# Kernel tuning notes

Hardware: AMD Instinct MI355X
Metric: run time of the kernel (lower is better)

## Reference

```python
import jax, jax.numpy as jnp
import numpy as np

EMBED_DIM = 1024
NUM_HEADS = 16
HEAD_DIM = EMBED_DIM // NUM_HEADS
B, SQ, SKV = 2, 2048, 2048


def setup_inputs() -> dict:
    key = jax.random.key(0)
    ks = jax.random.split(key, 12)
    s = 1.0 / np.sqrt(EMBED_DIM)
    inp = {
        "query": jax.random.normal(ks[0], (B, SQ, EMBED_DIM), jnp.float32),
        "key": jax.random.normal(ks[1], (B, SKV, EMBED_DIM), jnp.float32),
        "value": jax.random.normal(ks[2], (B, SKV, EMBED_DIM), jnp.float32),
        "Wq": jax.random.normal(ks[3], (EMBED_DIM, EMBED_DIM), jnp.float32) * s,
        "bq": jnp.zeros((EMBED_DIM,), jnp.float32),
        "Wk": jax.random.normal(ks[4], (EMBED_DIM, EMBED_DIM), jnp.float32) * s,
        "bk": jnp.zeros((EMBED_DIM,), jnp.float32),
        "Wv": jax.random.normal(ks[5], (EMBED_DIM, EMBED_DIM), jnp.float32) * s,
        "bv": jnp.zeros((EMBED_DIM,), jnp.float32),
        "Wo": jax.random.normal(ks[6], (EMBED_DIM, EMBED_DIM), jnp.float32) * s,
        "bo": jnp.zeros((EMBED_DIM,), jnp.float32),
        "ln_gamma": jnp.ones((EMBED_DIM,), jnp.float32),
        "ln_beta": jnp.zeros((EMBED_DIM,), jnp.float32),
    }
    return inp


def reference(query, key, value, Wq, bq, Wk, bk, Wv, bv, Wo, bo, ln_gamma, ln_beta):
    b, sq, d = query.shape
    skv = key.shape[1]
    residual = query
    # projections -> [b, h, s, hd]
    Q = (query @ Wq + bq).reshape(b, sq, NUM_HEADS, HEAD_DIM).transpose(0, 2, 1, 3)
    K = (key @ Wk + bk).reshape(b, skv, NUM_HEADS, HEAD_DIM).transpose(0, 2, 1, 3)
    V = (value @ Wv + bv).reshape(b, skv, NUM_HEADS, HEAD_DIM).transpose(0, 2, 1, 3)
    scores = jnp.einsum("bhqd,bhkd->bhqk", Q, K) / jnp.sqrt(jnp.float32(HEAD_DIM)).astype(Q.dtype)
    attn = jax.nn.softmax(scores, axis=-1)  # dropout identity in eval
    attended = jnp.einsum("bhqk,bhkd->bhqd", attn, V)
    attended = attended.transpose(0, 2, 1, 3).reshape(b, sq, d)
    out = attended @ Wo + bo
    x = out + residual
    mu = jnp.mean(x, axis=-1, keepdims=True)
    var = jnp.var(x, axis=-1, keepdims=True)
    return (x - mu) / jnp.sqrt(var + 1e-5) * ln_gamma + ln_beta
```

## Files before the change

kernel.cpp:

```cpp
#include <hip/hip_runtime.h>

#define EMBED 1024
#define NHEAD 16
#define HDIM  64
#define BATCH 2
#define SEQ   2048
#define ROWS  (BATCH*SEQ)

typedef __bf16 bf16x8 __attribute__((ext_vector_type(8)));
typedef float  f32x4  __attribute__((ext_vector_type(4)));
typedef float  f32x16 __attribute__((ext_vector_type(16)));
typedef unsigned short u16x8 __attribute__((ext_vector_type(8)));
typedef unsigned short u16x4 __attribute__((ext_vector_type(4)));

__device__ __forceinline__ unsigned short f2bf(float f) {
    unsigned int u = __float_as_uint(f);
    u += 0x7FFFu + ((u >> 16) & 1u);
    return (unsigned short)(u >> 16);
}
__device__ __forceinline__ f32x4 zero4() { f32x4 z = {0.f, 0.f, 0.f, 0.f}; return z; }

__device__ __forceinline__ unsigned int cvtpk_bf16(float lo, float hi) {
    unsigned int r;
    asm("v_cvt_pk_bf16_f32 %0, %1, %2" : "=v"(r) : "v"(lo), "v"(hi));
    return r;
}
__device__ __forceinline__ void pl32swap(unsigned int &a, unsigned int &b) {
    asm("v_permlane32_swap_b32 %0, %1" : "+v"(a), "+v"(b));
}
__device__ __forceinline__ float exp2_hw(float x) {
    float r;
    asm("v_exp_f32 %0, %1" : "=v"(r) : "v"(x));
    return r;
}

__device__ __forceinline__ void gl_lds16(const unsigned short* g, unsigned short* l) {
    __builtin_amdgcn_global_load_lds(
        (const __attribute__((address_space(1))) void*)g,
        (__attribute__((address_space(3))) void*)l, 16, 0, 0);
}

__global__ __launch_bounds__(256) void cvt3_kernel(const float* __restrict__ q,
                                                   const float* __restrict__ k,
                                                   const float* __restrict__ v,
                                                   unsigned short* __restrict__ qo,
                                                   unsigned short* __restrict__ ko,
                                                   unsigned short* __restrict__ vo) {
    const float* in; unsigned short* out;
    if (blockIdx.y == 0)      { in = q; out = qo; }
    else if (blockIdx.y == 1) { in = k; out = ko; }
    else                      { in = v; out = vo; }
    int i = (blockIdx.x * 256 + threadIdx.x) * 4;
    float4 vv = *(const float4*)(in + i);
    u16x4 o = {f2bf(vv.x), f2bf(vv.y), f2bf(vv.z), f2bf(vv.w)};
    *(u16x4*)(out + i) = o;
}

__global__ __launch_bounds__(256) void transpose4_kernel(const float* __restrict__ w0,
                                                         const float* __restrict__ w1,
                                                         const float* __restrict__ w2,
                                                         const float* __restrict__ w3,
                                                         unsigned short* __restrict__ o0,
                                                         unsigned short* __restrict__ o1,
                                                         unsigned short* __restrict__ o2,
                                                         unsigned short* __restrict__ o3) {
    const float* in; unsigned short* out;
    if (blockIdx.z == 0)      { in = w0; out = o0; }
    else if (blockIdx.z == 1) { in = w1; out = o1; }
    else if (blockIdx.z == 2) { in = w2; out = o2; }
    else                      { in = w3; out = o3; }
    __shared__ float tile[32][33];
    int tx = threadIdx.x, ty = threadIdx.y;
    int x = blockIdx.x * 32 + tx;
    int y0 = blockIdx.y * 32 + ty;
#pragma unroll
    for (int r = 0; r < 4; ++r)
        tile[ty + 8 * r][tx] = in[(size_t)(y0 + 8 * r) * EMBED + x];
    __syncthreads();
    int ox = blockIdx.y * 32 + tx;
    int oy = blockIdx.x * 32 + ty;
#pragma unroll
    for (int r = 0; r < 4; ++r)
        out[(size_t)(oy + 8 * r) * EMBED + ox] = f2bf(tile[tx][ty + 8 * r]);
}

__global__ __launch_bounds__(256, 2) void gemm_qkv_kernel(
    const unsigned short* __restrict__ qb, const unsigned short* __restrict__ kb,
    const unsigned short* __restrict__ vb,
    const unsigned short* __restrict__ Wqt, const unsigned short* __restrict__ Wkt,
    const unsigned short* __restrict__ Wvt,
    const float* __restrict__ bq, const float* __restrict__ bk, const float* __restrict__ bv,
    unsigned short* __restrict__ Qp, unsigned short* __restrict__ Kp,
    unsigned short* __restrict__ Vtb) {
    __shared__ unsigned short smem[24576];
    const unsigned short *A, *Bt; const float* bias; unsigned short* outp; int mode; float osc;
    if (blockIdx.z == 0)      { A = qb; Bt = Wqt; bias = bq; outp = Qp;  mode = 0; osc = 0.18033688f; }
    else if (blockIdx.z == 1) { A = kb; Bt = Wkt; bias = bk; outp = Kp;  mode = 0; osc = 1.0f; }
    else                      { A = vb; Bt = Wvt; bias = bv; outp = Vtb; mode = 1; osc = 1.0f; }

    const int t = threadIdx.x;
    const int m0 = blockIdx.x * 128, n0 = blockIdx.y * 128;
    const int wave = t >> 6, lane = t & 63;
    const int wr = wave >> 1, wc = wave & 1;
    const int lm = lane & 15, lq = lane >> 4;
    const int sr = t >> 2;
    const int csrc = (t & 3) ^ ((sr >> 1) & 3);
    const int pa = lq ^ ((lm >> 1) & 3);

    const unsigned short* gA = A + (size_t)(m0 + sr) * EMBED + csrc * 8;
    const unsigned short* gB = Bt + (size_t)(n0 + sr) * EMBED + csrc * 8;

    f32x4 acc[4][4];
#pragma unroll
    for (int i = 0; i < 4; ++i)
#pragma unroll
        for (int j = 0; j < 4; ++j) acc[i][j] = zero4();

#define QKV_STAGE(SOFF)                                                      \
    gl_lds16(gA,              smem + (SOFF) + wave * 512);                   \
    gl_lds16(gA + 64 * EMBED, smem + (SOFF) + 2048 + wave * 512);            \
    gl_lds16(gB,              smem + 12288 + (SOFF) + wave * 512);           \
    gl_lds16(gB + 64 * EMBED, smem + 12288 + (SOFF) + 2048 + wave * 512);    \
    gA += 32; gB += 32;

#define QKV_COMP(COFF)                                                                 \
    {                                                                                  \
        bf16x8 af[4], bfr[4];                                                          \
        _Pragma("unroll")                                                              \
        for (int i = 0; i < 4; ++i)                                                    \
            af[i] = *(const bf16x8*)&smem[(COFF) + (wr * 64 + i * 16 + lm) * 32 + pa * 8]; \
        _Pragma("unroll")                                                              \
        for (int j = 0; j < 4; ++j)                                                    \
            bfr[j] = *(const bf16x8*)&smem[12288 + (COFF) + (wc * 64 + j * 16 + lm) * 32 + pa * 8]; \
        _Pragma("unroll")                                                              \
        for (int i = 0; i < 4; ++i)                                                    \
            _Pragma("unroll")                                                          \
            for (int j = 0; j < 4; ++j)                                                \
                acc[i][j] = __builtin_amdgcn_mfma_f32_16x16x32_bf16(af[i], bfr[j], acc[i][j], 0, 0, 0); \
    }

    QKV_STAGE(0)
    QKV_STAGE(4096)

    for (int g = 0; g < 10; ++g) {
        asm volatile("s_waitcnt vmcnt(4)" ::: "memory");
        __builtin_amdgcn_s_barrier();
        QKV_STAGE(8192)
        QKV_COMP(0)
        asm volatile("s_waitcnt vmcnt(4)" ::: "memory");
        __builtin_amdgcn_s_barrier();
        QKV_STAGE(0)
        QKV_COMP(4096)
        asm volatile("s_waitcnt vmcnt(4)" ::: "memory");
        __builtin_amdgcn_s_barrier();
        QKV_STAGE(4096)
        QKV_COMP(8192)
    }
    asm volatile("s_waitcnt vmcnt(4)" ::: "memory");
    __builtin_amdgcn_s_barrier();
    QKV_COMP(0)
    asm volatile("s_waitcnt vmcnt(0)" ::: "memory");
    __builtin_amdgcn_s_barrier();
    QKV_COMP(4096)

    const int row = t >> 2, seg = t & 3;
    if (mode == 0) {
#pragma unroll
        for (int p = 0; p < 2; ++p) {
            __syncthreads();
            if (wr == p) {
#pragma unroll
                for (int i = 0; i < 4; ++i)
#pragma unroll
                    for (int j = 0; j < 4; ++j) {
                        float bn = bias[n0 + wc * 64 + j * 16 + lm];
                        int nl = wc * 64 + j * 16 + lm;
#pragma unroll
                        for (int r = 0; r < 4; ++r)
                            smem[(i * 16 + lq * 4 + r) * 136 + nl] =
                                f2bf((acc[i][j][r] + bn) * osc);
                    }
            }
            __syncthreads();
            int m = m0 + p * 64 + row;
            int b = m >> 11, sI = m & 2047;
            int ncol = n0 + seg * 32;
            int h = ncol >> 6, hd0 = ncol & 63;
            unsigned short* dst = outp + (((size_t)((b * NHEAD + h) * SEQ + sI)) << 6) + hd0;
            const unsigned short* src = smem + row * 136 + seg * 32;
            *(u16x8*)(dst)      = *(const u16x8*)(src);
            *(u16x8*)(dst + 8)  = *(const u16x8*)(src + 8);
            *(u16x8*)(dst + 16) = *(const u16x8*)(src + 16);
            *(u16x8*)(dst + 24) = *(const u16x8*)(src + 24);
        }
    } else {
#pragma unroll
        for (int p = 0; p < 2; ++p) {
            __syncthreads();
            if (wc == p) {
#pragma unroll
                for (int i = 0; i < 4; ++i)
#pragma unroll
                    for (int j = 0; j < 4; ++j) {
                        float bn = bias[n0 + p * 64 + j * 16 + lm];
                        u16x4 pw = {f2bf(acc[i][j][0] + bn), f2bf(acc[i][j][1] + bn),
                                    f2bf(acc[i][j][2] + bn), f2bf(acc[i][j][3] + bn)};
                        *(u16x4*)&smem[(j * 16 + lm) * 136 + wr * 64 + i * 16 + lq * 4] = pw;
                    }
            }
            __syncthreads();
            int n = n0 + p * 64 + row;
            int h = n >> 6, hd = n & 63;
            int b = m0 >> 11;
            int s0 = (m0 & 2047) + seg * 32;
            unsigned short* dst = outp + ((size_t)((b * NHEAD + h) * HDIM + hd)) * SEQ + s0;
            const unsigned short* src = smem + row * 136 + seg * 32;
            *(u16x8*)(dst)      = *(const u16x8*)(src);
            *(u16x8*)(dst + 8)  = *(const u16x8*)(src + 8);
            *(u16x8*)(dst + 16) = *(const u16x8*)(src + 16);
            *(u16x8*)(dst + 24) = *(const u16x8*)(src + 24);
        }
    }
#undef QKV_STAGE
#undef QKV_COMP
}

__global__ __launch_bounds__(256, 2) void gemm_o_kernel(
    const unsigned short* __restrict__ att, const unsigned short* __restrict__ Wot,
    const float* __restrict__ bo, float* __restrict__ xbuf,
    const float* __restrict__ residual) {
    __shared__ unsigned short smem[18432];
    const int t = threadIdx.x;
    const int m0 = blockIdx.x * 64, n0 = blockIdx.y * 128;
    const int wave = t >> 6, lane = t & 63;
    const int lm = lane & 15, lq = lane >> 4;
    const int sr = t >> 2;
    const int csrc = (t & 3) ^ ((sr >> 1) & 3);
    const int pa = lq ^ ((lm >> 1) & 3);

    const unsigned short* gA = att + (size_t)(m0 + sr) * EMBED + csrc * 8;
    const unsigned short* gB = Wot + (size_t)(n0 + sr) * EMBED + csrc * 8;

    f32x4 acc[4][2];
#pragma unroll
    for (int i = 0; i < 4; ++i)
#pragma unroll
        for (int j = 0; j < 2; ++j) acc[i][j] = zero4();

#define O_STAGE(SA, SB)                                                  \
    gl_lds16(gA,              smem + (SA) + wave * 512);                 \
    gl_lds16(gB,              smem + 6144 + (SB) + wave * 512);          \
    gl_lds16(gB + 64 * EMBED, smem + 6144 + (SB) + 2048 + wave * 512);   \
    gA += 32; gB += 32;

#define O_COMP(SA, SB)                                                                \
    {                                                                                 \
        bf16x8 af[4], bfr[2];                                                         \
        _Pragma("unroll")                                                             \
        for (int i = 0; i < 4; ++i)                                                   \
            af[i] = *(const bf16x8*)&smem[(SA) + (i * 16 + lm) * 32 + pa * 8];        \
        _Pragma("unroll")                                                             \
        for (int j = 0; j < 2; ++j)                                                   \
            bfr[j] = *(const bf16x8*)&smem[6144 + (SB) + (wave * 32 + j * 16 + lm) * 32 + pa * 8]; \
        _Pragma("unroll")                                                             \
        for (int i = 0; i < 4; ++i)                                                   \
            _Pragma("unroll")                                                         \
            for (int j = 0; j < 2; ++j)                                               \
                acc[i][j] = __builtin_amdgcn_mfma_f32_16x16x32_bf16(af[i], bfr[j], acc[i][j], 0, 0, 0); \
    }

    O_STAGE(0, 0)
    O_STAGE(2048, 4096)

    for (int g = 0; g < 10; ++g) {
        asm volatile("s_waitcnt vmcnt(3)" ::: "memory");
        __builtin_amdgcn_s_barrier();
        O_STAGE(4096, 8192)
        O_COMP(0, 0)
        asm volatile("s_waitcnt vmcnt(3)" ::: "memory");
        __builtin_amdgcn_s_barrier();
        O_STAGE(0, 0)
        O_COMP(2048, 4096)
        asm volatile("s_waitcnt vmcnt(3)" ::: "memory");
        __builtin_amdgcn_s_barrier();
        O_STAGE(2048, 4096)
        O_COMP(4096, 8192)
    }
    asm volatile("s_waitcnt vmcnt(3)" ::: "memory");
    __builtin_amdgcn_s_barrier();
    O_COMP(0, 0)
    asm volatile("s_waitcnt vmcnt(0)" ::: "memory");
    __builtin_amdgcn_s_barrier();
    O_COMP(2048, 4096)

#pragma unroll
    for (int i = 0; i < 4; ++i)
#pragma unroll
        for (int j = 0; j < 2; ++j) {
            int n = n0 + wave * 32 + j * 16 + lm;
            float bn = bo[n];
#pragma unroll
            for (int r = 0; r < 4; ++r) {
                int m = m0 + i * 16 + lq * 4 + r;
                size_t idx = (size_t)m * EMBED + n;
                xbuf[idx] = acc[i][j][r] + bn + residual[idx];
            }
        }
#undef O_STAGE
#undef O_COMP
}

__global__ __launch_bounds__(512, 4) void attn_kernel(const unsigned short* __restrict__ Qp,
                                                      const unsigned short* __restrict__ Kp,
                                                      const unsigned short* __restrict__ Vt,
                                                      unsigned short* __restrict__ att) {
    __shared__ unsigned short KV[32768];
    unsigned short* Ks = KV;
    unsigned short* Vs = KV + 16384;
    const int t = threadIdx.x;
    const int bx = blockIdx.x;
    const int bh = bx & 31;
    const int b = bh >> 4, h = bh & 15;
    const int q0 = (bx >> 5) * 128;
    const unsigned short* Qh = Qp + (size_t)bh * SEQ * HDIM;
    const unsigned short* Kh = Kp + (size_t)bh * SEQ * HDIM;
    const unsigned short* Vh = Vt + (size_t)bh * HDIM * SEQ;
    const int wave = t >> 6, lane = t & 63;
    const int g = wave >> 2, ws = wave & 3;
    const int ln31 = lane & 31, halfl = lane >> 5;

    bf16x8 qf[4];
    {
        const unsigned short* qptr = Qh + (size_t)(q0 + ws * 32 + ln31) * HDIM + halfl * 8;
#pragma unroll
        for (int s = 0; s < 4; ++s) qf[s] = *(const bf16x8*)(qptr + s * 16);
    }

    const int f0 = t >> 6, m0_ = t & 31, hh0 = (t >> 5) & 1;
    const unsigned short* gK0 = Kh + (size_t)((f0 >> 2) * 32 + m0_) * HDIM + (f0 & 3) * 16 + hh0 * 8;
    const unsigned short* gV0 = Vh + (size_t)((f0 >> 2) * 32 + m0_) * SEQ + (f0 & 3) * 16 + hh0 * 8;

#define ATTN_STAGE(NBO)                                                   \
    gl_lds16(gK0,             Ks + (NBO) + wave * 512);                   \
    gl_lds16(gK0 + 64 * HDIM, Ks + (NBO) + 4096 + wave * 512);            \
    gl_lds16(gV0,             Vs + (NBO) + wave * 512);                   \
    gl_lds16(gV0 + 64,        Vs + (NBO) + 4096 + wave * 512);            \
    gK0 += 128 * HDIM; gV0 += 128;

    ATTN_STAGE(0)
    ATTN_STAGE(8192)

    f32x16 OFFS;
#pragma unroll
    for (int r = 0; r < 16; ++r) OFFS[r] = -17.312340f;

    f32x16 Oa[2];
#pragma unroll
    for (int mo = 0; mo < 2; ++mo)
#pragma unroll
        for (int r = 0; r < 16; ++r) Oa[mo][r] = 0.f;
    float rpA = 0.f, rpB = 0.f, rpC = 0.f, rpD = 0.f;

    for (int kt = 0; kt < 16; ++kt) {
        if (kt < 15) { asm volatile("s_waitcnt vmcnt(4)" ::: "memory"); }
        else         { asm volatile("s_waitcnt vmcnt(0)" ::: "memory"); }
        __builtin_amdgcn_s_barrier();
        const int cbo = (kt & 1) * 8192 + g * 4096;

#pragma unroll
        for (int mt = 0; mt < 2; ++mt) {
            f32x16 S;
            __builtin_amdgcn_s_setprio(1);
            {
                bf16x8 af = *(const bf16x8*)&Ks[cbo + (mt * 4 + 0) * 512 + halfl * 256 + ln31 * 8];
                S = __builtin_amdgcn_mfma_f32_32x32x16_bf16(af, qf[0], OFFS, 0, 0, 0);
            }
#pragma unroll
            for (int s = 1; s < 4; ++s) {
                bf16x8 af = *(const bf16x8*)&Ks[cbo + (mt * 4 + s) * 512 + halfl * 256 + ln31 * 8];
                S = __builtin_amdgcn_mfma_f32_32x32x16_bf16(af, qf[s], S, 0, 0, 0);
            }
            __builtin_amdgcn_s_setprio(0);

#pragma unroll
            for (int rg = 0; rg < 4; ++rg) {
                float p0 = exp2_hw(S[rg * 4 + 0]);
                float p1 = exp2_hw(S[rg * 4 + 1]);
                float p2 = exp2_hw(S[rg * 4 + 2]);
                float p3 = exp2_hw(S[rg * 4 + 3]);
                S[rg * 4 + 0] = p0; rpA += p0;
                S[rg * 4 + 1] = p1; rpB += p1;
                S[rg * 4 + 2] = p2; rpC += p2;
                S[rg * 4 + 3] = p3; rpD += p3;
            }

            __builtin_amdgcn_s_setprio(1);
#pragma unroll
            for (int p = 0; p < 2; ++p) {
                unsigned int a0 = cvtpk_bf16(S[8 * p + 0], S[8 * p + 1]);
                unsigned int a1 = cvtpk_bf16(S[8 * p + 2], S[8 * p + 3]);
                unsigned int b0 = cvtpk_bf16(S[8 * p + 4], S[8 * p + 5]);
                unsigned int b1 = cvtpk_bf16(S[8 * p + 6], S[8 * p + 7]);
                pl32swap(a0, b0);
                pl32swap(a1, b1);
                union { unsigned int u[4]; bf16x8 v; } bp;
                bp.u[0] = a0; bp.u[1] = a1; bp.u[2] = b0; bp.u[3] = b1;
                const int sp = mt * 2 + p;
#pragma unroll
                for (int mo = 0; mo < 2; ++mo) {
                    bf16x8 av = *(const bf16x8*)&Vs[cbo + (mo * 4 + sp) * 512 + halfl * 256 + ln31 * 8];
                    Oa[mo] = __builtin_amdgcn_mfma_f32_32x32x16_bf16(av, bp.v, Oa[mo], 0, 0, 0);
                }
            }
            __builtin_amdgcn_s_setprio(0);
        }

        if (kt < 14) {
            __builtin_amdgcn_s_barrier();
            const int nbo = (kt & 1) * 8192;
            ATTN_STAGE(nbo)
        }
    }
#undef ATTN_STAGE

    float lsum = (rpA + rpB) + (rpC + rpD);
    unsigned int la = __float_as_uint(lsum), lb = __float_as_uint(lsum);
    pl32swap(la, lb);
    float ltot = __uint_as_float(la) + __uint_as_float(lb);

    __syncthreads();
    float* shO = (float*)KV;
    float* shL = (float*)KV + 128 * 68;
    const int qr = ws * 32 + ln31;
    if (g == 1) {
#pragma unroll
        for (int mo = 0; mo < 2; ++mo)
#pragma unroll
            for (int rg = 0; rg < 4; ++rg) {
                float4 v;
                v.x = Oa[mo][rg * 4 + 0]; v.y = Oa[mo][rg * 4 + 1];
                v.z = Oa[mo][rg * 4 + 2]; v.w = Oa[mo][rg * 4 + 3];
                *(float4*)&shO[qr * 68 + mo * 32 + rg * 8 + halfl * 4] = v;
            }
        shL[qr] = ltot;
    }
    __syncthreads();
    if (g == 0) {
        float inv = 1.f / (ltot + shL[qr]);
        unsigned short* orow = att + (size_t)(b * SEQ + q0 + qr) * EMBED + h * HDIM;
#pragma unroll
        for (int mo = 0; mo < 2; ++mo)
#pragma unroll
            for (int rg = 0; rg < 4; ++rg) {
                float4 v = *(const float4*)&shO[qr * 68 + mo * 32 + rg * 8 + halfl * 4];
                u16x4 ow = {f2bf((Oa[mo][rg * 4 + 0] + v.x) * inv),
                            f2bf((Oa[mo][rg * 4 + 1] + v.y) * inv),
                            f2bf((Oa[mo][rg * 4 + 2] + v.z) * inv),
                            f2bf((Oa[mo][rg * 4 + 3] + v.w) * inv)};
                *(u16x4*)&orow[mo * 32 + rg * 8 + halfl * 4] = ow;
            }
    }
}

__global__ __launch_bounds__(256) void ln_kernel(const float* __restrict__ x,
                                                 const float* __restrict__ gamma,
                                                 const float* __restrict__ beta,
                                                 float* __restrict__ out) {
    __shared__ float red[8];
    const int row = blockIdx.x, t = threadIdx.x;
    float4 v = *(const float4*)(x + (size_t)row * EMBED + t * 4);
    float s = v.x + v.y + v.z + v.w;
    float ss = v.x * v.x + v.y * v.y + v.z * v.z + v.w * v.w;
#pragma unroll
    for (int o = 1; o < 64; o <<= 1) {
        s += __shfl_xor(s, o);
        ss += __shfl_xor(ss, o);
    }
    int wave = t >> 6, lane = t & 63;
    if (lane == 0) { red[wave] = s; red[4 + wave] = ss; }
    __syncthreads();
    s = red[0] + red[1] + red[2] + red[3];
    ss = red[4] + red[5] + red[6] + red[7];
    float mu = s * (1.f / EMBED);
    float var = ss * (1.f / EMBED) - mu * mu;
    float rstd = rsqrtf(var + 1e-5f);
    float4 g = *(const float4*)(gamma + t * 4);
    float4 bb = *(const float4*)(beta + t * 4);
    float4 o;
    o.x = (v.x - mu) * rstd * g.x + bb.x;
    o.y = (v.y - mu) * rstd * g.y + bb.y;
    o.z = (v.z - mu) * rstd * g.z + bb.z;
    o.w = (v.w - mu) * rstd * g.w + bb.w;
    *(float4*)(out + (size_t)row * EMBED + t * 4) = o;
}

extern "C" void kernel_launch(void* const* d_in, const int* in_sizes, int n_in,
                              void* d_out, int out_size, void* d_ws, size_t ws_size,
                              hipStream_t stream) {
    const float* query = (const float*)d_in[0];
    const float* key_  = (const float*)d_in[1];
    const float* value = (const float*)d_in[2];
    const float* Wq = (const float*)d_in[3];
    const float* bq = (const float*)d_in[4];
    const float* Wk = (const float*)d_in[5];
    const float* bk = (const float*)d_in[6];
    const float* Wv = (const float*)d_in[7];
    const float* bv = (const float*)d_in[8];
    const float* Wo = (const float*)d_in[9];
    const float* bo = (const float*)d_in[10];
    const float* gamma = (const float*)d_in[11];
    const float* beta  = (const float*)d_in[12];

    char* ws = (char*)d_ws;
    const size_t MB = 1024 * 1024;
    unsigned short* qb  = (unsigned short*)(ws + 0);
    unsigned short* kb  = (unsigned short*)(ws + 8 * MB);
    unsigned short* vb  = (unsigned short*)(ws + 16 * MB);
    unsigned short* Wqt = (unsigned short*)(ws + 24 * MB);
    unsigned short* Wkt = (unsigned short*)(ws + 26 * MB);
    unsigned short* Wvt = (unsigned short*)(ws + 28 * MB);
    unsigned short* Wot = (unsigned short*)(ws + 30 * MB);
    unsigned short* Qp  = (unsigned short*)(ws + 32 * MB);
    unsigned short* Kp  = (unsigned short*)(ws + 40 * MB);
    unsigned short* Vtb = (unsigned short*)(ws + 48 * MB);
    unsigned short* att = (unsigned short*)(ws + 0);
    float*          xbuf = (float*)(ws + 8 * MB);

    cvt3_kernel<<<dim3(4096, 3), 256, 0, stream>>>(query, key_, value, qb, kb, vb);
    transpose4_kernel<<<dim3(32, 32, 4), dim3(32, 8), 0, stream>>>(Wq, Wk, Wv, Wo, Wqt, Wkt, Wvt, Wot);

    gemm_qkv_kernel<<<dim3(32, 8, 3), 256, 0, stream>>>(qb, kb, vb, Wqt, Wkt, Wvt,
                                                        bq, bk, bv, Qp, Kp, Vtb);

    attn_kernel<<<dim3(512), 512, 0, stream>>>(Qp, Kp, Vtb, att);

    gemm_o_kernel<<<dim3(64, 8), 256, 0, stream>>>(att, Wot, bo, xbuf, query);
    ln_kernel<<<ROWS, 256, 0, stream>>>(xbuf, gamma, beta, (float*)d_out);
}
```

Baseline: 224.9 us.

## Split-K the output projection GEMM and fold bias/residual into LayerNorm

The output projection GEMM is split into two K halves via a z grid dimension, doubling the block count from 512 to 1024 so the GPU's compute units have more blocks to run. Each half writes raw partial sums to a separate fp32 buffer, and the LayerNorm kernel now adds both partials, the bias and the residual. This adds an extra 16 MB fp32 write plus read of partials. Separately, the input conversion kernel handles 8 elements per thread with wider stores.

```diff
diff --git a/kernel.cpp b/kernel.cpp
--- a/kernel.cpp
+++ b/kernel.cpp
@@ -50,10 +50,12 @@
     if (blockIdx.y == 0)      { in = q; out = qo; }
     else if (blockIdx.y == 1) { in = k; out = ko; }
     else                      { in = v; out = vo; }
-    int i = (blockIdx.x * 256 + threadIdx.x) * 4;
-    float4 vv = *(const float4*)(in + i);
-    u16x4 o = {f2bf(vv.x), f2bf(vv.y), f2bf(vv.z), f2bf(vv.w)};
-    *(u16x4*)(out + i) = o;
+    int i = (blockIdx.x * 256 + threadIdx.x) * 8;
+    float4 a = *(const float4*)(in + i);
+    float4 b = *(const float4*)(in + i + 4);
+    u16x8 o = {f2bf(a.x), f2bf(a.y), f2bf(a.z), f2bf(a.w),
+               f2bf(b.x), f2bf(b.y), f2bf(b.z), f2bf(b.w)};
+    *(u16x8*)(out + i) = o;
 }
 
 __global__ __launch_bounds__(256) void transpose4_kernel(const float* __restrict__ w0,
@@ -227,19 +229,20 @@
 
 __global__ __launch_bounds__(256, 2) void gemm_o_kernel(
     const unsigned short* __restrict__ att, const unsigned short* __restrict__ Wot,
-    const float* __restrict__ bo, float* __restrict__ xbuf,
-    const float* __restrict__ residual) {
+    float* __restrict__ xbuf0, float* __restrict__ xbuf1) {
     __shared__ unsigned short smem[18432];
     const int t = threadIdx.x;
     const int m0 = blockIdx.x * 64, n0 = blockIdx.y * 128;
+    const int kz = blockIdx.z;
+    float* outp = kz ? xbuf1 : xbuf0;
     const int wave = t >> 6, lane = t & 63;
     const int lm = lane & 15, lq = lane >> 4;
     const int sr = t >> 2;
     const int csrc = (t & 3) ^ ((sr >> 1) & 3);
     const int pa = lq ^ ((lm >> 1) & 3);
 
-    const unsigned short* gA = att + (size_t)(m0 + sr) * EMBED + csrc * 8;
-    const unsigned short* gB = Wot + (size_t)(n0 + sr) * EMBED + csrc * 8;
+    const unsigned short* gA = att + (size_t)(m0 + sr) * EMBED + kz * 512 + csrc * 8;
+    const unsigned short* gB = Wot + (size_t)(n0 + sr) * EMBED + kz * 512 + csrc * 8;
 
     f32x4 acc[4][2];
 #pragma unroll
@@ -272,7 +275,7 @@
     O_STAGE(0, 0)
     O_STAGE(2048, 4096)
 
-    for (int g = 0; g < 10; ++g) {
+    for (int g = 0; g < 4; ++g) {
         asm volatile("s_waitcnt vmcnt(3)" ::: "memory");
         __builtin_amdgcn_s_barrier();
         O_STAGE(4096, 8192)
@@ -288,22 +291,28 @@
     }
     asm volatile("s_waitcnt vmcnt(3)" ::: "memory");
     __builtin_amdgcn_s_barrier();
+    O_STAGE(4096, 8192)
     O_COMP(0, 0)
+    asm volatile("s_waitcnt vmcnt(3)" ::: "memory");
+    __builtin_amdgcn_s_barrier();
+    O_STAGE(0, 0)
+    O_COMP(2048, 4096)
+    asm volatile("s_waitcnt vmcnt(3)" ::: "memory");
+    __builtin_amdgcn_s_barrier();
+    O_COMP(4096, 8192)
     asm volatile("s_waitcnt vmcnt(0)" ::: "memory");
     __builtin_amdgcn_s_barrier();
-    O_COMP(2048, 4096)
+    O_COMP(0, 0)
 
 #pragma unroll
     for (int i = 0; i < 4; ++i)
 #pragma unroll
         for (int j = 0; j < 2; ++j) {
             int n = n0 + wave * 32 + j * 16 + lm;
-            float bn = bo[n];
 #pragma unroll
             for (int r = 0; r < 4; ++r) {
                 int m = m0 + i * 16 + lq * 4 + r;
-                size_t idx = (size_t)m * EMBED + n;
-                xbuf[idx] = acc[i][j][r] + bn + residual[idx];
+                outp[(size_t)m * EMBED + n] = acc[i][j][r];
             }
         }
 #undef O_STAGE
@@ -462,13 +471,25 @@
     }
 }
 
-__global__ __launch_bounds__(256) void ln_kernel(const float* __restrict__ x,
+__global__ __launch_bounds__(256) void ln_kernel(const float* __restrict__ x0,
+                                                 const float* __restrict__ x1,
+                                                 const float* __restrict__ residual,
+                                                 const float* __restrict__ bo,
                                                  const float* __restrict__ gamma,
                                                  const float* __restrict__ beta,
                                                  float* __restrict__ out) {
     __shared__ float red[8];
     const int row = blockIdx.x, t = threadIdx.x;
-    float4 v = *(const float4*)(x + (size_t)row * EMBED + t * 4);
+    size_t base = (size_t)row * EMBED + t * 4;
+    float4 a = *(const float4*)(x0 + base);
+    float4 c = *(const float4*)(x1 + base);
+    float4 r = *(const float4*)(residual + base);
+    float4 bb0 = *(const float4*)(bo + t * 4);
+    float4 v;
+    v.x = a.x + c.x + bb0.x + r.x;
+    v.y = a.y + c.y + bb0.y + r.y;
+    v.z = a.z + c.z + bb0.z + r.z;
+    v.w = a.w + c.w + bb0.w + r.w;
     float s = v.x + v.y + v.z + v.w;
     float ss = v.x * v.x + v.y * v.y + v.z * v.z + v.w * v.w;
 #pragma unroll
@@ -524,9 +545,10 @@
     unsigned short* Kp  = (unsigned short*)(ws + 40 * MB);
     unsigned short* Vtb = (unsigned short*)(ws + 48 * MB);
     unsigned short* att = (unsigned short*)(ws + 0);
-    float*          xbuf = (float*)(ws + 8 * MB);
-
-    cvt3_kernel<<<dim3(4096, 3), 256, 0, stream>>>(query, key_, value, qb, kb, vb);
+    float*          xbuf0 = (float*)(ws + 8 * MB);
+    float*          xbuf1 = (float*)(ws + 32 * MB);
+
+    cvt3_kernel<<<dim3(2048, 3), 256, 0, stream>>>(query, key_, value, qb, kb, vb);
     transpose4_kernel<<<dim3(32, 32, 4), dim3(32, 8), 0, stream>>>(Wq, Wk, Wv, Wo, Wqt, Wkt, Wvt, Wot);
 
     gemm_qkv_kernel<<<dim3(32, 8, 3), 256, 0, stream>>>(qb, kb, vb, Wqt, Wkt, Wvt,
@@ -534,6 +556,6 @@
 
     attn_kernel<<<dim3(512), 512, 0, stream>>>(Qp, Kp, Vtb, att);
 
-    gemm_o_kernel<<<dim3(64, 8), 256, 0, stream>>>(att, Wot, bo, xbuf, query);
-    ln_kernel<<<ROWS, 256, 0, stream>>>(xbuf, gamma, beta, (float*)d_out);
-}
+    gemm_o_kernel<<<dim3(64, 8, 2), 256, 0, stream>>>(att, Wot, xbuf0, xbuf1);
+    ln_kernel<<<ROWS, 256, 0, stream>>>(xbuf0, xbuf1, query, bo, gamma, beta, (float*)d_out);
+}
```

Measured after the change: 227.3 us. About the same (+1.1%).

## Merge input-cast and weight-transpose kernels; hoist both QK^T tiles before softmax

Applied to the files above, without the earlier changes.

The separate fp32->bf16 cast kernel and the weight transpose kernel are merged into one launch that splits its 1D grid by block index. The cast path now handles 8 elements per thread. In the attention loop, both 32-key score tiles (S0, S1) are now computed before any exp/PV work, so the second QK^T MFMA chain can overlap with the softmax of the first. This saves one launch and exposes more independent MFMA work, at the cost of holding more accumulator registers live.

```diff
diff --git a/kernel.cpp b/kernel.cpp
--- a/kernel.cpp
+++ b/kernel.cpp
@@ -40,48 +40,52 @@
         (__attribute__((address_space(3))) void*)l, 16, 0, 0);
 }
 
-__global__ __launch_bounds__(256) void cvt3_kernel(const float* __restrict__ q,
-                                                   const float* __restrict__ k,
-                                                   const float* __restrict__ v,
-                                                   unsigned short* __restrict__ qo,
-                                                   unsigned short* __restrict__ ko,
-                                                   unsigned short* __restrict__ vo) {
-    const float* in; unsigned short* out;
-    if (blockIdx.y == 0)      { in = q; out = qo; }
-    else if (blockIdx.y == 1) { in = k; out = ko; }
-    else                      { in = v; out = vo; }
-    int i = (blockIdx.x * 256 + threadIdx.x) * 4;
-    float4 vv = *(const float4*)(in + i);
-    u16x4 o = {f2bf(vv.x), f2bf(vv.y), f2bf(vv.z), f2bf(vv.w)};
-    *(u16x4*)(out + i) = o;
-}
-
-__global__ __launch_bounds__(256) void transpose4_kernel(const float* __restrict__ w0,
-                                                         const float* __restrict__ w1,
-                                                         const float* __restrict__ w2,
-                                                         const float* __restrict__ w3,
-                                                         unsigned short* __restrict__ o0,
-                                                         unsigned short* __restrict__ o1,
-                                                         unsigned short* __restrict__ o2,
-                                                         unsigned short* __restrict__ o3) {
-    const float* in; unsigned short* out;
-    if (blockIdx.z == 0)      { in = w0; out = o0; }
-    else if (blockIdx.z == 1) { in = w1; out = o1; }
-    else if (blockIdx.z == 2) { in = w2; out = o2; }
-    else                      { in = w3; out = o3; }
+__global__ __launch_bounds__(256) void prep_kernel(
+    const float* __restrict__ q, const float* __restrict__ k, const float* __restrict__ v,
+    unsigned short* __restrict__ qo, unsigned short* __restrict__ ko,
+    unsigned short* __restrict__ vo,
+    const float* __restrict__ w0, const float* __restrict__ w1,
+    const float* __restrict__ w2, const float* __restrict__ w3,
+    unsigned short* __restrict__ o0, unsigned short* __restrict__ o1,
+    unsigned short* __restrict__ o2, unsigned short* __restrict__ o3) {
     __shared__ float tile[32][33];
-    int tx = threadIdx.x, ty = threadIdx.y;
-    int x = blockIdx.x * 32 + tx;
-    int y0 = blockIdx.y * 32 + ty;
-#pragma unroll
-    for (int r = 0; r < 4; ++r)
-        tile[ty + 8 * r][tx] = in[(size_t)(y0 + 8 * r) * EMBED + x];
-    __syncthreads();
-    int ox = blockIdx.y * 32 + tx;
-    int oy = blockIdx.x * 32 + ty;
-#pragma unroll
-    for (int r = 0; r < 4; ++r)
-        out[(size_t)(oy + 8 * r) * EMBED + ox] = f2bf(tile[tx][ty + 8 * r]);
+    const int bx = blockIdx.x, t = threadIdx.x;
+    if (bx < 6144) {
+        const float* in; unsigned short* out;
+        int m = bx >> 11;
+        int blk = bx & 2047;
+        if (m == 0)      { in = q; out = qo; }
+        else if (m == 1) { in = k; out = ko; }
+        else             { in = v; out = vo; }
+        int i = (blk * 256 + t) * 8;
+        float4 a = *(const float4*)(in + i);
+        float4 b = *(const float4*)(in + i + 4);
+        u16x8 o = {f2bf(a.x), f2bf(a.y), f2bf(a.z), f2bf(a.w),
+                   f2bf(b.x), f2bf(b.y), f2bf(b.z), f2bf(b.w)};
+        *(u16x8*)(out + i) = o;
+    } else {
+        int idx = bx - 6144;
+        int z = idx >> 10;
+        int rem = idx & 1023;
+        int bxx = rem & 31, byy = rem >> 5;
+        const float* in; unsigned short* out;
+        if (z == 0)      { in = w0; out = o0; }
+        else if (z == 1) { in = w1; out = o1; }
+        else if (z == 2) { in = w2; out = o2; }
+        else             { in = w3; out = o3; }
+        int tx = t & 31, ty = t >> 5;
+        int x = bxx * 32 + tx;
+        int y0 = byy * 32 + ty;
+#pragma unroll
+        for (int r = 0; r < 4; ++r)
+            tile[ty + 8 * r][tx] = in[(size_t)(y0 + 8 * r) * EMBED + x];
+        __syncthreads();
+        int ox = byy * 32 + tx;
+        int oy = bxx * 32 + ty;
+#pragma unroll
+        for (int r = 0; r < 4; ++r)
+            out[(size_t)(oy + 8 * r) * EMBED + ox] = f2bf(tile[tx][ty + 8 * r]);
+    }
 }
 
 __global__ __launch_bounds__(256, 2) void gemm_qkv_kernel(
@@ -367,53 +371,65 @@
         __builtin_amdgcn_s_barrier();
         const int cbo = (kt & 1) * 8192 + g * 4096;
 
-#pragma unroll
-        for (int mt = 0; mt < 2; ++mt) {
-            f32x16 S;
-            __builtin_amdgcn_s_setprio(1);
-            {
-                bf16x8 af = *(const bf16x8*)&Ks[cbo + (mt * 4 + 0) * 512 + halfl * 256 + ln31 * 8];
-                S = __builtin_amdgcn_mfma_f32_32x32x16_bf16(af, qf[0], OFFS, 0, 0, 0);
-            }
-#pragma unroll
-            for (int s = 1; s < 4; ++s) {
-                bf16x8 af = *(const bf16x8*)&Ks[cbo + (mt * 4 + s) * 512 + halfl * 256 + ln31 * 8];
-                S = __builtin_amdgcn_mfma_f32_32x32x16_bf16(af, qf[s], S, 0, 0, 0);
-            }
-            __builtin_amdgcn_s_setprio(0);
-
-#pragma unroll
-            for (int rg = 0; rg < 4; ++rg) {
-                float p0 = exp2_hw(S[rg * 4 + 0]);
-                float p1 = exp2_hw(S[rg * 4 + 1]);
-                float p2 = exp2_hw(S[rg * 4 + 2]);
-                float p3 = exp2_hw(S[rg * 4 + 3]);
-                S[rg * 4 + 0] = p0; rpA += p0;
-                S[rg * 4 + 1] = p1; rpB += p1;
-                S[rg * 4 + 2] = p2; rpC += p2;
-                S[rg * 4 + 3] = p3; rpD += p3;
-            }
-
-            __builtin_amdgcn_s_setprio(1);
-#pragma unroll
-            for (int p = 0; p < 2; ++p) {
-                unsigned int a0 = cvtpk_bf16(S[8 * p + 0], S[8 * p + 1]);
-                unsigned int a1 = cvtpk_bf16(S[8 * p + 2], S[8 * p + 3]);
-                unsigned int b0 = cvtpk_bf16(S[8 * p + 4], S[8 * p + 5]);
-                unsigned int b1 = cvtpk_bf16(S[8 * p + 6], S[8 * p + 7]);
-                pl32swap(a0, b0);
-                pl32swap(a1, b1);
-                union { unsigned int u[4]; bf16x8 v; } bp;
-                bp.u[0] = a0; bp.u[1] = a1; bp.u[2] = b0; bp.u[3] = b1;
-                const int sp = mt * 2 + p;
-#pragma unroll
-                for (int mo = 0; mo < 2; ++mo) {
-                    bf16x8 av = *(const bf16x8*)&Vs[cbo + (mo * 4 + sp) * 512 + halfl * 256 + ln31 * 8];
-                    Oa[mo] = __builtin_amdgcn_mfma_f32_32x32x16_bf16(av, bp.v, Oa[mo], 0, 0, 0);
-                }
-            }
-            __builtin_amdgcn_s_setprio(0);
-        }
+        f32x16 S0, S1;
+        __builtin_amdgcn_s_setprio(1);
+        {
+            bf16x8 af = *(const bf16x8*)&Ks[cbo + halfl * 256 + ln31 * 8];
+            S0 = __builtin_amdgcn_mfma_f32_32x32x16_bf16(af, qf[0], OFFS, 0, 0, 0);
+        }
+#pragma unroll
+        for (int s = 1; s < 4; ++s) {
+            bf16x8 af = *(const bf16x8*)&Ks[cbo + s * 512 + halfl * 256 + ln31 * 8];
+            S0 = __builtin_amdgcn_mfma_f32_32x32x16_bf16(af, qf[s], S0, 0, 0, 0);
+        }
+        {
+            bf16x8 af = *(const bf16x8*)&Ks[cbo + 4 * 512 + halfl * 256 + ln31 * 8];
+            S1 = __builtin_amdgcn_mfma_f32_32x32x16_bf16(af, qf[0], OFFS, 0, 0, 0);
+        }
+#pragma unroll
+        for (int s = 1; s < 4; ++s) {
+            bf16x8 af = *(const bf16x8*)&Ks[cbo + (4 + s) * 512 + halfl * 256 + ln31 * 8];
+            S1 = __builtin_amdgcn_mfma_f32_32x32x16_bf16(af, qf[s], S1, 0, 0, 0);
+        }
+        __builtin_amdgcn_s_setprio(0);
+
+#define SMPV(S, MT)                                                               \
+        {                                                                         \
+            _Pragma("unroll")                                                     \
+            for (int rg = 0; rg < 4; ++rg) {                                      \
+                float p0 = exp2_hw(S[rg * 4 + 0]);                                \
+                float p1 = exp2_hw(S[rg * 4 + 1]);                                \
+                float p2 = exp2_hw(S[rg * 4 + 2]);                                \
+                float p3 = exp2_hw(S[rg * 4 + 3]);                                \
+                S[rg * 4 + 0] = p0; rpA += p0;                                    \
+                S[rg * 4 + 1] = p1; rpB += p1;                                    \
+                S[rg * 4 + 2] = p2; rpC += p2;                                    \
+                S[rg * 4 + 3] = p3; rpD += p3;                                    \
+            }                                                                     \
+            __builtin_amdgcn_s_setprio(1);                                        \
+            _Pragma("unroll")                                                     \
+            for (int p = 0; p < 2; ++p) {                                         \
+                unsigned int a0 = cvtpk_bf16(S[8 * p + 0], S[8 * p + 1]);         \
+                unsigned int a1 = cvtpk_bf16(S[8 * p + 2], S[8 * p + 3]);         \
+                unsigned int b0 = cvtpk_bf16(S[8 * p + 4], S[8 * p + 5]);         \
+                unsigned int b1 = cvtpk_bf16(S[8 * p + 6], S[8 * p + 7]);         \
+                pl32swap(a0, b0);                                                 \
+                pl32swap(a1, b1);                                                 \
+                union { unsigned int u[4]; bf16x8 v; } bp;                        \
+                bp.u[0] = a0; bp.u[1] = a1; bp.u[2] = b0; bp.u[3] = b1;           \
+                const int sp = (MT) * 2 + p;                                      \
+                _Pragma("unroll")                                                 \
+                for (int mo = 0; mo < 2; ++mo) {                                  \
+                    bf16x8 av = *(const bf16x8*)&Vs[cbo + (mo * 4 + sp) * 512 + halfl * 256 + ln31 * 8]; \
+                    Oa[mo] = __builtin_amdgcn_mfma_f32_32x32x16_bf16(av, bp.v, Oa[mo], 0, 0, 0); \
+                }                                                                 \
+            }                                                                     \
+            __builtin_amdgcn_s_setprio(0);                                        \
+        }
+
+        SMPV(S0, 0)
+        SMPV(S1, 1)
+#undef SMPV
 
         if (kt < 14) {
             __builtin_amdgcn_s_barrier();
@@ -526,8 +542,8 @@
     unsigned short* att = (unsigned short*)(ws + 0);
     float*          xbuf = (float*)(ws + 8 * MB);
 
-    cvt3_kernel<<<dim3(4096, 3), 256, 0, stream>>>(query, key_, value, qb, kb, vb);
-    transpose4_kernel<<<dim3(32, 32, 4), dim3(32, 8), 0, stream>>>(Wq, Wk, Wv, Wo, Wqt, Wkt, Wvt, Wot);
+    prep_kernel<<<dim3(10240), 256, 0, stream>>>(query, key_, value, qb, kb, vb,
+                                                 Wq, Wk, Wv, Wo, Wqt, Wkt, Wvt, Wot);
 
     gemm_qkv_kernel<<<dim3(32, 8, 3), 256, 0, stream>>>(qb, kb, vb, Wqt, Wkt, Wvt,
                                                         bq, bk, bv, Qp, Kp, Vtb);
```

Measured after the change: 223.9 us. About the same (-0.4%).
